# Optimization experiments

Hardware: AMD Instinct MI355X
Metric: run time of the kernel (lower is better)

Reference implementation:

```python
import jax, jax.numpy as jnp
import numpy as np

K_BITS = 128  # hash bits (k in __init__)
WORD = 32     # pack bits into uint32 words -> K_BITS // WORD = 4 words


def _pack_bits(bits_u32):
    # bits_u32: [N, K_BITS] uint32 in {0,1} -> [N, K_BITS//WORD] uint32 keys
    N = bits_u32.shape[0]
    b = bits_u32.reshape(N, K_BITS // WORD, WORD)
    shifts = jnp.arange(WORD, dtype=jnp.uint32)
    return jnp.sum(jnp.left_shift(b, shifts), axis=-1, dtype=jnp.uint32)  # [N, 4]


def setup_inputs() -> dict:
    key = jax.random.key(0)
    k1, k2 = jax.random.split(key)
    T, B, D = 128, 64, 4096
    latent_state = jax.random.normal(k1, (T, B, D), dtype=jnp.float32)
    A = jax.random.normal(k2, (K_BITS, D), dtype=jnp.float32)  # fixed random projection buffer
    return {"latent_state": latent_state, "A": A}


def reference(latent_state, A):
    # latent_state: [T, B, D]; A: [k, D]. Returns intrinsic reward [T, B].
    T, B, D = latent_state.shape
    flat = latent_state.reshape(T * B, D)                    # detach is a no-op for fwd
    proj = flat @ A.T                                        # [N, k]
    bits = (proj > 0).astype(jnp.uint32)                     # SimHash sign bits
    words = _pack_bits(bits)                                 # [N, 4] collision-free 128-bit key

    # counts dict starts empty each run: visit count of row i is the number of
    # rows j <= i with an identical key (keys processed in row order).
    N = words.shape[0]
    eq = jnp.ones((N, N), dtype=bool)
    for w in range(K_BITS // WORD):  # small fixed loop over 4 key words
        eq = eq & (words[:, None, w] == words[None, :, w])
    counts = jnp.tril(eq).sum(axis=1)                        # [N] int, >= 1
    intrinsic = 1.0 / jnp.sqrt(counts.astype(latent_state.dtype))
    return intrinsic.reshape(T, B)
```

## Files before the change

kernel.cpp:

```cpp
#include <hip/hip_runtime.h>
#include <stdint.h>

#define D_DIM 4096
#define N_ROWS 8192

typedef __attribute__((ext_vector_type(8))) short bfrag8;
typedef __attribute__((ext_vector_type(4))) float facc4;
typedef unsigned long long u64;

__device__ __forceinline__ uint32_t pack_bf16x2(float lo, float hi) {
    union { float f; uint32_t u; } a, b;
    a.f = lo; b.f = hi;
    return (b.u & 0xFFFF0000u) | (a.u >> 16);
}

__global__ void __launch_bounds__(256)
prep_A(const float* __restrict__ A, uint32_t* __restrict__ A_sw) {
    const int S = blockIdx.x * 256 + threadIdx.x;
    const int c = S >> 10;
    const int s = S & 1023;
    const int n = s >> 3;
    const int g = (s & 7) ^ (n & 7);
    const float* src = A + (size_t)n * D_DIM + c * 64 + g * 8;
    float4 f0 = *(const float4*)(src);
    float4 f1 = *(const float4*)(src + 4);
    uint4 o;
    o.x = pack_bf16x2(f0.x, f0.y);
    o.y = pack_bf16x2(f0.z, f0.w);
    o.z = pack_bf16x2(f1.x, f1.y);
    o.w = pack_bf16x2(f1.z, f1.w);
    *(uint4*)(A_sw + (size_t)S * 4) = o;
}

__global__ void __launch_bounds__(256)
gemm_split(const float* __restrict__ L, const uint32_t* __restrict__ A_sw,
           float* __restrict__ partials, int kpb) {
    __shared__ ushort Ls[32 * 72];
    __shared__ uint4 As[1024];

    const int tid  = threadIdx.x;
    const int wave = tid >> 6;
    const int lane = tid & 63;
    const int split = blockIdx.x;
    const int row0 = blockIdx.y * 32;
    const int c  = lane & 15;
    const int q  = lane >> 4;
    const int wm = wave >> 1;
    const int wn = wave & 1;

    const int lrow = tid >> 3;
    const int lf4  = tid & 7;
    const float* lsrc = L + (size_t)(row0 + lrow) * D_DIM + lf4 * 4;
    ushort* ldst = &Ls[lrow * 72 + lf4 * 4];

    facc4 acc[4];
#pragma unroll
    for (int i = 0; i < 4; i++) acc[i] = (facc4){0.f, 0.f, 0.f, 0.f};

    const int kc0 = split * kpb * 64;
    const int kc1 = kc0 + kpb * 64;
    for (int kc = kc0; kc < kc1; kc += 64) {
        const uint32_t* gA = A_sw + (size_t)(kc >> 6) * 4096;
#pragma unroll
        for (int i = 0; i < 4; i++) {
            const int slot0 = wave * 256 + i * 64;
            __builtin_amdgcn_global_load_lds(
                (const __attribute__((address_space(1))) uint32_t*)(gA + (slot0 + lane) * 4),
                (__attribute__((address_space(3))) uint32_t*)(&As[slot0]),
                16, 0, 0);
        }
        float4 f0 = *(const float4*)(lsrc + kc);
        float4 f1 = *(const float4*)(lsrc + kc + 32);
        *(uint2*)ldst        = make_uint2(pack_bf16x2(f0.x, f0.y), pack_bf16x2(f0.z, f0.w));
        *(uint2*)(ldst + 32) = make_uint2(pack_bf16x2(f1.x, f1.y), pack_bf16x2(f1.z, f1.w));
        __syncthreads();

#pragma unroll
        for (int ks = 0; ks < 2; ks++) {
            bfrag8 a = *(const bfrag8*)&Ls[(16 * wm + c) * 72 + ks * 32 + q * 8];
#pragma unroll
            for (int ct = 0; ct < 4; ct++) {
                const int n  = 64 * wn + 16 * ct + c;
                const int gl = ks * 4 + q;
                bfrag8 b = *(const bfrag8*)&As[n * 8 + (gl ^ (n & 7))];
                acc[ct] = __builtin_amdgcn_mfma_f32_16x16x32_bf16(a, b, acc[ct], 0, 0, 0);
            }
        }
        __syncthreads();
    }

    float* P = partials + ((size_t)split * N_ROWS * 128);
    const int rb = row0 + 16 * wm + 4 * q;
    const int cb = 64 * wn + c;
#pragma unroll
    for (int ct = 0; ct < 4; ct++)
#pragma unroll
        for (int r = 0; r < 4; r++)
            P[(size_t)(rb + r) * 128 + cb + 16 * ct] = acc[ct][r];
}

__global__ void __launch_bounds__(256)
reduce_pack(const float* __restrict__ partials, u64* __restrict__ folded, int S) {
    const int row  = blockIdx.x * 4 + (threadIdx.x >> 6);
    const int lane = threadIdx.x & 63;
    float s0 = 0.f, s1 = 0.f;
    for (int s = 0; s < S; s++) {
        const float* P = partials + ((size_t)s * N_ROWS * 128) + (size_t)row * 128;
        s0 += P[lane];
        s1 += P[lane + 64];
    }
    u64 b0 = __ballot(s0 > 0.0f);
    u64 b1 = __ballot(s1 > 0.0f);
    if (lane == 0) folded[row] = b0 ^ b1;
}

__global__ void __launch_bounds__(256)
gemm_pack(const float* __restrict__ L, const uint32_t* __restrict__ A_sw,
          u64* __restrict__ folded) {
    __shared__ ushort Ls[32 * 72];
    __shared__ uint4 As[1024];
    __shared__ u64 halves[2][32];

    const int tid  = threadIdx.x;
    const int wave = tid >> 6;
    const int lane = tid & 63;
    const int row0 = blockIdx.x * 32;
    const int c  = lane & 15;
    const int q  = lane >> 4;
    const int wm = wave >> 1;
    const int wn = wave & 1;

    const int lrow = tid >> 3;
    const int lf4  = tid & 7;
    const float* lsrc = L + (size_t)(row0 + lrow) * D_DIM + lf4 * 4;
    ushort* ldst = &Ls[lrow * 72 + lf4 * 4];

    facc4 acc[4];
#pragma unroll
    for (int i = 0; i < 4; i++) acc[i] = (facc4){0.f, 0.f, 0.f, 0.f};

    for (int kc = 0; kc < D_DIM; kc += 64) {
        const uint32_t* gA = A_sw + (size_t)(kc >> 6) * 4096;
#pragma unroll
        for (int i = 0; i < 4; i++) {
            const int slot0 = wave * 256 + i * 64;
            __builtin_amdgcn_global_load_lds(
                (const __attribute__((address_space(1))) uint32_t*)(gA + (slot0 + lane) * 4),
                (__attribute__((address_space(3))) uint32_t*)(&As[slot0]),
                16, 0, 0);
        }
        float4 f0 = *(const float4*)(lsrc + kc);
        float4 f1 = *(const float4*)(lsrc + kc + 32);
        *(uint2*)ldst        = make_uint2(pack_bf16x2(f0.x, f0.y), pack_bf16x2(f0.z, f0.w));
        *(uint2*)(ldst + 32) = make_uint2(pack_bf16x2(f1.x, f1.y), pack_bf16x2(f1.z, f1.w));
        __syncthreads();

#pragma unroll
        for (int ks = 0; ks < 2; ks++) {
            bfrag8 a = *(const bfrag8*)&Ls[(16 * wm + c) * 72 + ks * 32 + q * 8];
#pragma unroll
            for (int ct = 0; ct < 4; ct++) {
                const int n  = 64 * wn + 16 * ct + c;
                const int gl = ks * 4 + q;
                bfrag8 b = *(const bfrag8*)&As[n * 8 + (gl ^ (n & 7))];
                acc[ct] = __builtin_amdgcn_mfma_f32_16x16x32_bf16(a, b, acc[ct], 0, 0, 0);
            }
        }
        __syncthreads();
    }

    u64 masks[4][4];
#pragma unroll
    for (int ct = 0; ct < 4; ct++)
#pragma unroll
        for (int r = 0; r < 4; r++)
            masks[ct][r] = __ballot(acc[ct][r] > 0.0f);

    if (lane < 16) {
        const int qq = lane >> 2, r = lane & 3;
        u64 half = 0;
#pragma unroll
        for (int ct = 0; ct < 4; ct++) {
            u64 bits = (masks[ct][r] >> (16 * qq)) & 0xFFFFull;
            half |= bits << (16 * ct);
        }
        halves[wn][16 * wm + lane] = half;
    }
    __syncthreads();
    if (tid < 32)
        folded[row0 + tid] = halves[0][tid] ^ halves[1][tid];
}

__global__ void __launch_bounds__(512)
count_rows(const u64* __restrict__ folded, float* __restrict__ out) {
    __shared__ u64 K[N_ROWS];
    const int tid = threadIdx.x;
    for (int i = tid; i < N_ROWS; i += 512) K[i] = folded[i];
    __syncthreads();

    const int g    = blockIdx.x * 8 + (tid >> 6);
    const int lane = tid & 63;
    int rows[4];
    u64 my[4];
    int cnt[4] = {0, 0, 0, 0};
#pragma unroll
    for (int r = 0; r < 4; r++) {
        rows[r] = g + 2048 * r;
        my[r] = K[rows[r]];
    }
    const int maxrow = rows[3];
    for (int j = lane; j <= maxrow; j += 64) {
        u64 k = K[j];
#pragma unroll
        for (int r = 0; r < 4; r++)
            cnt[r] += (int)((j <= rows[r]) & (k == my[r]));
    }
#pragma unroll
    for (int r = 0; r < 4; r++) {
        int v = cnt[r];
#pragma unroll
        for (int o = 32; o; o >>= 1) v += __shfl_xor(v, o, 64);
        if (lane == 0) out[rows[r]] = rsqrtf((float)v);
    }
}

extern "C" void kernel_launch(void* const* d_in, const int* in_sizes, int n_in,
                              void* d_out, int out_size, void* d_ws, size_t ws_size,
                              hipStream_t stream) {
    const float* latent = (const float*)d_in[0];
    const float* A      = (const float*)d_in[1];
    float* out          = (float*)d_out;

    uint32_t* A_sw = (uint32_t*)d_ws;
    u64* folded = (u64*)((char*)d_ws + (1 << 20));
    float* partials = (float*)((char*)d_ws + (1 << 20) + (1 << 16));

    const size_t base = (1 << 20) + (1 << 16);
    const size_t per_split = (size_t)N_ROWS * 128 * sizeof(float);
    int S = 0;
    if (ws_size >= base + 8 * per_split)      S = 8;
    else if (ws_size >= base + 4 * per_split) S = 4;
    else if (ws_size >= base + 2 * per_split) S = 2;

    prep_A<<<256, 256, 0, stream>>>(A, A_sw);
    if (S > 0) {
        gemm_split<<<dim3(S, 256), 256, 0, stream>>>(latent, A_sw, partials, 64 / S);
        reduce_pack<<<2048, 256, 0, stream>>>(partials, folded, S);
    } else {
        gemm_pack<<<256, 256, 0, stream>>>(latent, A_sw, folded);
    }
    count_rows<<<256, 512, 0, stream>>>(folded, out);
}
```

Measured before the change: 225.8 us.

## Fuse split-K GEMM and reduction into one 1024-thread block with LDS reduce

Replaces the split-K GEMM, which wrote fp32 partials to global memory and needed a separate reduce_pack kernel, with one kernel per 32-row tile. Inside it, four 256-thread groups each handle a quarter of K and combine their accumulators through shared memory before packing the sign bits. This removes the partials round-trip through global memory and one kernel launch. The price is a 1024-thread block with four copies of the LDS buffers, which may limit occupancy, and only 256 blocks in the grid.

```diff
diff --git a/kernel.cpp b/kernel.cpp
--- a/kernel.cpp
+++ b/kernel.cpp
@@ -32,41 +32,41 @@
     *(uint4*)(A_sw + (size_t)S * 4) = o;
 }
 
-__global__ void __launch_bounds__(256)
-gemm_split(const float* __restrict__ L, const uint32_t* __restrict__ A_sw,
-           float* __restrict__ partials, int kpb) {
-    __shared__ ushort Ls[32 * 72];
-    __shared__ uint4 As[1024];
+__global__ void __launch_bounds__(1024, 4)
+gemm_pack_fused(const float* __restrict__ L, const uint32_t* __restrict__ A_sw,
+                u64* __restrict__ folded) {
+    __shared__ ushort Ls[4][32 * 72];
+    __shared__ uint4  As[4][1024];
+    __shared__ u64 halves[2][32];
 
     const int tid  = threadIdx.x;
-    const int wave = tid >> 6;
+    const int g    = tid >> 8;
+    const int t    = tid & 255;
+    const int wg   = t >> 6;
     const int lane = tid & 63;
-    const int split = blockIdx.x;
-    const int row0 = blockIdx.y * 32;
+    const int row0 = blockIdx.x * 32;
     const int c  = lane & 15;
     const int q  = lane >> 4;
-    const int wm = wave >> 1;
-    const int wn = wave & 1;
+    const int wm = wg >> 1;
+    const int wn = wg & 1;
 
-    const int lrow = tid >> 3;
-    const int lf4  = tid & 7;
-    const float* lsrc = L + (size_t)(row0 + lrow) * D_DIM + lf4 * 4;
-    ushort* ldst = &Ls[lrow * 72 + lf4 * 4];
+    const int lrow = t >> 3;
+    const int lf4  = t & 7;
+    const float* lsrc = L + (size_t)(row0 + lrow) * D_DIM + g * 1024 + lf4 * 4;
+    ushort* ldst = &Ls[g][lrow * 72 + lf4 * 4];
 
     facc4 acc[4];
 #pragma unroll
     for (int i = 0; i < 4; i++) acc[i] = (facc4){0.f, 0.f, 0.f, 0.f};
 
-    const int kc0 = split * kpb * 64;
-    const int kc1 = kc0 + kpb * 64;
-    for (int kc = kc0; kc < kc1; kc += 64) {
-        const uint32_t* gA = A_sw + (size_t)(kc >> 6) * 4096;
+    for (int kc = 0; kc < 1024; kc += 64) {
+        const uint32_t* gA = A_sw + (size_t)((g * 1024 + kc) >> 6) * 4096;
 #pragma unroll
         for (int i = 0; i < 4; i++) {
-            const int slot0 = wave * 256 + i * 64;
+            const int slot0 = wg * 256 + i * 64;
             __builtin_amdgcn_global_load_lds(
                 (const __attribute__((address_space(1))) uint32_t*)(gA + (slot0 + lane) * 4),
-                (__attribute__((address_space(3))) uint32_t*)(&As[slot0]),
+                (__attribute__((address_space(3))) uint32_t*)(&As[g][slot0]),
                 16, 0, 0);
         }
         float4 f0 = *(const float4*)(lsrc + kc);
@@ -77,114 +77,52 @@
 
 #pragma unroll
         for (int ks = 0; ks < 2; ks++) {
-            bfrag8 a = *(const bfrag8*)&Ls[(16 * wm + c) * 72 + ks * 32 + q * 8];
+            bfrag8 a = *(const bfrag8*)&Ls[g][(16 * wm + c) * 72 + ks * 32 + q * 8];
 #pragma unroll
             for (int ct = 0; ct < 4; ct++) {
                 const int n  = 64 * wn + 16 * ct + c;
                 const int gl = ks * 4 + q;
-                bfrag8 b = *(const bfrag8*)&As[n * 8 + (gl ^ (n & 7))];
+                bfrag8 b = *(const bfrag8*)&As[g][n * 8 + (gl ^ (n & 7))];
                 acc[ct] = __builtin_amdgcn_mfma_f32_16x16x32_bf16(a, b, acc[ct], 0, 0, 0);
             }
         }
         __syncthreads();
     }
 
-    float* P = partials + ((size_t)split * N_ROWS * 128);
-    const int rb = row0 + 16 * wm + 4 * q;
-    const int cb = 64 * wn + c;
+    facc4* red = (facc4*)&As[0][0];
+    const int sw = (t >> 1) & 7;
+    if (g > 0) {
+        facc4* dst = red + (g - 1) * 1024;
 #pragma unroll
-    for (int ct = 0; ct < 4; ct++)
+        for (int ct = 0; ct < 4; ct++)
+            dst[(t * 4 + ct) ^ sw] = acc[ct];
+    }
+    __syncthreads();
+    if (g == 0) {
 #pragma unroll
-        for (int r = 0; r < 4; r++)
-            P[(size_t)(rb + r) * 128 + cb + 16 * ct] = acc[ct][r];
-}
+        for (int s = 0; s < 3; s++) {
+            const facc4* src = red + s * 1024;
+#pragma unroll
+            for (int ct = 0; ct < 4; ct++)
+                acc[ct] += src[(t * 4 + ct) ^ sw];
+        }
+        u64 masks[4][4];
+#pragma unroll
+        for (int ct = 0; ct < 4; ct++)
+#pragma unroll
+            for (int r = 0; r < 4; r++)
+                masks[ct][r] = __ballot(acc[ct][r] > 0.0f);
 
-__global__ void __launch_bounds__(256)
-reduce_pack(const float* __restrict__ partials, u64* __restrict__ folded, int S) {
-    const int row  = blockIdx.x * 4 + (threadIdx.x >> 6);
-    const int lane = threadIdx.x & 63;
-    float s0 = 0.f, s1 = 0.f;
-    for (int s = 0; s < S; s++) {
-        const float* P = partials + ((size_t)s * N_ROWS * 128) + (size_t)row * 128;
-        s0 += P[lane];
-        s1 += P[lane + 64];
-    }
-    u64 b0 = __ballot(s0 > 0.0f);
-    u64 b1 = __ballot(s1 > 0.0f);
-    if (lane == 0) folded[row] = b0 ^ b1;
-}
-
-__global__ void __launch_bounds__(256)
-gemm_pack(const float* __restrict__ L, const uint32_t* __restrict__ A_sw,
-          u64* __restrict__ folded) {
-    __shared__ ushort Ls[32 * 72];
-    __shared__ uint4 As[1024];
-    __shared__ u64 halves[2][32];
-
-    const int tid  = threadIdx.x;
-    const int wave = tid >> 6;
-    const int lane = tid & 63;
-    const int row0 = blockIdx.x * 32;
-    const int c  = lane & 15;
-    const int q  = lane >> 4;
-    const int wm = wave >> 1;
-    const int wn = wave & 1;
-
-    const int lrow = tid >> 3;
-    const int lf4  = tid & 7;
-    const float* lsrc = L + (size_t)(row0 + lrow) * D_DIM + lf4 * 4;
-    ushort* ldst = &Ls[lrow * 72 + lf4 * 4];
-
-    facc4 acc[4];
-#pragma unroll
-    for (int i = 0; i < 4; i++) acc[i] = (facc4){0.f, 0.f, 0.f, 0.f};
-
-    for (int kc = 0; kc < D_DIM; kc += 64) {
-        const uint32_t* gA = A_sw + (size_t)(kc >> 6) * 4096;
-#pragma unroll
-        for (int i = 0; i < 4; i++) {
-            const int slot0 = wave * 256 + i * 64;
-            __builtin_amdgcn_global_load_lds(
-                (const __attribute__((address_space(1))) uint32_t*)(gA + (slot0 + lane) * 4),
-                (__attribute__((address_space(3))) uint32_t*)(&As[slot0]),
-                16, 0, 0);
-        }
-        float4 f0 = *(const float4*)(lsrc + kc);
-        float4 f1 = *(const float4*)(lsrc + kc + 32);
-        *(uint2*)ldst        = make_uint2(pack_bf16x2(f0.x, f0.y), pack_bf16x2(f0.z, f0.w));
-        *(uint2*)(ldst + 32) = make_uint2(pack_bf16x2(f1.x, f1.y), pack_bf16x2(f1.z, f1.w));
-        __syncthreads();
-
-#pragma unroll
-        for (int ks = 0; ks < 2; ks++) {
-            bfrag8 a = *(const bfrag8*)&Ls[(16 * wm + c) * 72 + ks * 32 + q * 8];
+        if (lane < 16) {
+            const int qq = lane >> 2, r = lane & 3;
+            u64 half = 0;
 #pragma unroll
             for (int ct = 0; ct < 4; ct++) {
-                const int n  = 64 * wn + 16 * ct + c;
-                const int gl = ks * 4 + q;
-                bfrag8 b = *(const bfrag8*)&As[n * 8 + (gl ^ (n & 7))];
-                acc[ct] = __builtin_amdgcn_mfma_f32_16x16x32_bf16(a, b, acc[ct], 0, 0, 0);
+                u64 bits = (masks[ct][r] >> (16 * qq)) & 0xFFFFull;
+                half |= bits << (16 * ct);
             }
+            halves[wn][16 * wm + lane] = half;
         }
-        __syncthreads();
-    }
-
-    u64 masks[4][4];
-#pragma unroll
-    for (int ct = 0; ct < 4; ct++)
-#pragma unroll
-        for (int r = 0; r < 4; r++)
-            masks[ct][r] = __ballot(acc[ct][r] > 0.0f);
-
-    if (lane < 16) {
-        const int qq = lane >> 2, r = lane & 3;
-        u64 half = 0;
-#pragma unroll
-        for (int ct = 0; ct < 4; ct++) {
-            u64 bits = (masks[ct][r] >> (16 * qq)) & 0xFFFFull;
-            half |= bits << (16 * ct);
-        }
-        halves[wn][16 * wm + lane] = half;
     }
     __syncthreads();
     if (tid < 32)
@@ -233,21 +171,8 @@
 
     uint32_t* A_sw = (uint32_t*)d_ws;
     u64* folded = (u64*)((char*)d_ws + (1 << 20));
-    float* partials = (float*)((char*)d_ws + (1 << 20) + (1 << 16));
-
-    const size_t base = (1 << 20) + (1 << 16);
-    const size_t per_split = (size_t)N_ROWS * 128 * sizeof(float);
-    int S = 0;
-    if (ws_size >= base + 8 * per_split)      S = 8;
-    else if (ws_size >= base + 4 * per_split) S = 4;
-    else if (ws_size >= base + 2 * per_split) S = 2;
 
     prep_A<<<256, 256, 0, stream>>>(A, A_sw);
-    if (S > 0) {
-        gemm_split<<<dim3(S, 256), 256, 0, stream>>>(latent, A_sw, partials, 64 / S);
-        reduce_pack<<<2048, 256, 0, stream>>>(partials, folded, S);
-    } else {
-        gemm_pack<<<256, 256, 0, stream>>>(latent, A_sw, folded);
-    }
+    gemm_pack_fused<<<256, 1024, 0, stream>>>(latent, A_sw, folded);
     count_rows<<<256, 512, 0, stream>>>(folded, out);
 }
```

Measured after the change: 228.7 us. No clear change (+1.3%).

## Enlarge split-K GEMM row tile to 128 rows to reuse A tile across rows

Applied to the files above, without the earlier changes.

The split-K projection GEMM now processes 128 latent rows per block instead of 32. Each wave computes a 4x4 grid of MFMA tiles, so every A fragment loaded from LDS is reused across four row tiles. This cuts how often the 128xK A chunk is reloaded per row, at the cost of more accumulator registers and a 4x smaller grid (S x 64 blocks), which may lower occupancy or parallelism. The fused non-split fallback is removed and S defaults to 1, so the split path always runs.

```diff
diff --git a/kernel.cpp b/kernel.cpp
--- a/kernel.cpp
+++ b/kernel.cpp
@@ -32,17 +32,17 @@
     *(uint4*)(A_sw + (size_t)S * 4) = o;
 }
 
-__global__ void __launch_bounds__(256)
-gemm_split(const float* __restrict__ L, const uint32_t* __restrict__ A_sw,
-           float* __restrict__ partials, int kpb) {
-    __shared__ ushort Ls[32 * 72];
-    __shared__ uint4 As[1024];
+__global__ void __launch_bounds__(256, 2)
+gemm_split128(const float* __restrict__ L, const uint32_t* __restrict__ A_sw,
+              float* __restrict__ partials, int kpb) {
+    __shared__ ushort Ls[128 * 72];
+    __shared__ uint4  As[1024];
 
     const int tid  = threadIdx.x;
     const int wave = tid >> 6;
     const int lane = tid & 63;
     const int split = blockIdx.x;
-    const int row0 = blockIdx.y * 32;
+    const int row0 = blockIdx.y * 128;
     const int c  = lane & 15;
     const int q  = lane >> 4;
     const int wm = wave >> 1;
@@ -53,9 +53,11 @@
     const float* lsrc = L + (size_t)(row0 + lrow) * D_DIM + lf4 * 4;
     ushort* ldst = &Ls[lrow * 72 + lf4 * 4];
 
-    facc4 acc[4];
+    facc4 acc[4][4];
 #pragma unroll
-    for (int i = 0; i < 4; i++) acc[i] = (facc4){0.f, 0.f, 0.f, 0.f};
+    for (int m = 0; m < 4; m++)
+#pragma unroll
+        for (int ct = 0; ct < 4; ct++) acc[m][ct] = (facc4){0.f, 0.f, 0.f, 0.f};
 
     const int kc0 = split * kpb * 64;
     const int kc1 = kc0 + kpb * 64;
@@ -69,34 +71,48 @@
                 (__attribute__((address_space(3))) uint32_t*)(&As[slot0]),
                 16, 0, 0);
         }
-        float4 f0 = *(const float4*)(lsrc + kc);
-        float4 f1 = *(const float4*)(lsrc + kc + 32);
-        *(uint2*)ldst        = make_uint2(pack_bf16x2(f0.x, f0.y), pack_bf16x2(f0.z, f0.w));
-        *(uint2*)(ldst + 32) = make_uint2(pack_bf16x2(f1.x, f1.y), pack_bf16x2(f1.z, f1.w));
+#pragma unroll
+        for (int i = 0; i < 4; i++) {
+            const float* p = lsrc + (size_t)i * 32 * D_DIM + kc;
+            float4 f0 = *(const float4*)(p);
+            float4 f1 = *(const float4*)(p + 32);
+            *(uint2*)(ldst + i * 32 * 72) =
+                make_uint2(pack_bf16x2(f0.x, f0.y), pack_bf16x2(f0.z, f0.w));
+            *(uint2*)(ldst + i * 32 * 72 + 32) =
+                make_uint2(pack_bf16x2(f1.x, f1.y), pack_bf16x2(f1.z, f1.w));
+        }
         __syncthreads();
 
 #pragma unroll
         for (int ks = 0; ks < 2; ks++) {
-            bfrag8 a = *(const bfrag8*)&Ls[(16 * wm + c) * 72 + ks * 32 + q * 8];
+            bfrag8 a[4];
+#pragma unroll
+            for (int m = 0; m < 4; m++)
+                a[m] = *(const bfrag8*)&Ls[(64 * wm + 16 * m + c) * 72 + ks * 32 + q * 8];
 #pragma unroll
             for (int ct = 0; ct < 4; ct++) {
                 const int n  = 64 * wn + 16 * ct + c;
                 const int gl = ks * 4 + q;
                 bfrag8 b = *(const bfrag8*)&As[n * 8 + (gl ^ (n & 7))];
-                acc[ct] = __builtin_amdgcn_mfma_f32_16x16x32_bf16(a, b, acc[ct], 0, 0, 0);
+#pragma unroll
+                for (int m = 0; m < 4; m++)
+                    acc[m][ct] = __builtin_amdgcn_mfma_f32_16x16x32_bf16(a[m], b, acc[m][ct], 0, 0, 0);
             }
         }
         __syncthreads();
     }
 
     float* P = partials + ((size_t)split * N_ROWS * 128);
-    const int rb = row0 + 16 * wm + 4 * q;
     const int cb = 64 * wn + c;
 #pragma unroll
-    for (int ct = 0; ct < 4; ct++)
+    for (int m = 0; m < 4; m++) {
+        const int rb = row0 + 64 * wm + 16 * m + 4 * q;
 #pragma unroll
-        for (int r = 0; r < 4; r++)
-            P[(size_t)(rb + r) * 128 + cb + 16 * ct] = acc[ct][r];
+        for (int ct = 0; ct < 4; ct++)
+#pragma unroll
+            for (int r = 0; r < 4; r++)
+                P[(size_t)(rb + r) * 128 + cb + 16 * ct] = acc[m][ct][r];
+    }
 }
 
 __global__ void __launch_bounds__(256)
@@ -112,83 +128,6 @@
     u64 b0 = __ballot(s0 > 0.0f);
     u64 b1 = __ballot(s1 > 0.0f);
     if (lane == 0) folded[row] = b0 ^ b1;
-}
-
-__global__ void __launch_bounds__(256)
-gemm_pack(const float* __restrict__ L, const uint32_t* __restrict__ A_sw,
-          u64* __restrict__ folded) {
-    __shared__ ushort Ls[32 * 72];
-    __shared__ uint4 As[1024];
-    __shared__ u64 halves[2][32];
-
-    const int tid  = threadIdx.x;
-    const int wave = tid >> 6;
-    const int lane = tid & 63;
-    const int row0 = blockIdx.x * 32;
-    const int c  = lane & 15;
-    const int q  = lane >> 4;
-    const int wm = wave >> 1;
-    const int wn = wave & 1;
-
-    const int lrow = tid >> 3;
-    const int lf4  = tid & 7;
-    const float* lsrc = L + (size_t)(row0 + lrow) * D_DIM + lf4 * 4;
-    ushort* ldst = &Ls[lrow * 72 + lf4 * 4];
-
-    facc4 acc[4];
-#pragma unroll
-    for (int i = 0; i < 4; i++) acc[i] = (facc4){0.f, 0.f, 0.f, 0.f};
-
-    for (int kc = 0; kc < D_DIM; kc += 64) {
-        const uint32_t* gA = A_sw + (size_t)(kc >> 6) * 4096;
-#pragma unroll
-        for (int i = 0; i < 4; i++) {
-            const int slot0 = wave * 256 + i * 64;
-            __builtin_amdgcn_global_load_lds(
-                (const __attribute__((address_space(1))) uint32_t*)(gA + (slot0 + lane) * 4),
-                (__attribute__((address_space(3))) uint32_t*)(&As[slot0]),
-                16, 0, 0);
-        }
-        float4 f0 = *(const float4*)(lsrc + kc);
-        float4 f1 = *(const float4*)(lsrc + kc + 32);
-        *(uint2*)ldst        = make_uint2(pack_bf16x2(f0.x, f0.y), pack_bf16x2(f0.z, f0.w));
-        *(uint2*)(ldst + 32) = make_uint2(pack_bf16x2(f1.x, f1.y), pack_bf16x2(f1.z, f1.w));
-        __syncthreads();
-
-#pragma unroll
-        for (int ks = 0; ks < 2; ks++) {
-            bfrag8 a = *(const bfrag8*)&Ls[(16 * wm + c) * 72 + ks * 32 + q * 8];
-#pragma unroll
-            for (int ct = 0; ct < 4; ct++) {
-                const int n  = 64 * wn + 16 * ct + c;
-                const int gl = ks * 4 + q;
-                bfrag8 b = *(const bfrag8*)&As[n * 8 + (gl ^ (n & 7))];
-                acc[ct] = __builtin_amdgcn_mfma_f32_16x16x32_bf16(a, b, acc[ct], 0, 0, 0);
-            }
-        }
-        __syncthreads();
-    }
-
-    u64 masks[4][4];
-#pragma unroll
-    for (int ct = 0; ct < 4; ct++)
-#pragma unroll
-        for (int r = 0; r < 4; r++)
-            masks[ct][r] = __ballot(acc[ct][r] > 0.0f);
-
-    if (lane < 16) {
-        const int qq = lane >> 2, r = lane & 3;
-        u64 half = 0;
-#pragma unroll
-        for (int ct = 0; ct < 4; ct++) {
-            u64 bits = (masks[ct][r] >> (16 * qq)) & 0xFFFFull;
-            half |= bits << (16 * ct);
-        }
-        halves[wn][16 * wm + lane] = half;
-    }
-    __syncthreads();
-    if (tid < 32)
-        folded[row0 + tid] = halves[0][tid] ^ halves[1][tid];
 }
 
 __global__ void __launch_bounds__(512)
@@ -237,17 +176,13 @@
 
     const size_t base = (1 << 20) + (1 << 16);
     const size_t per_split = (size_t)N_ROWS * 128 * sizeof(float);
-    int S = 0;
+    int S = 1;
     if (ws_size >= base + 8 * per_split)      S = 8;
     else if (ws_size >= base + 4 * per_split) S = 4;
     else if (ws_size >= base + 2 * per_split) S = 2;
 
     prep_A<<<256, 256, 0, stream>>>(A, A_sw);
-    if (S > 0) {
-        gemm_split<<<dim3(S, 256), 256, 0, stream>>>(latent, A_sw, partials, 64 / S);
-        reduce_pack<<<2048, 256, 0, stream>>>(partials, folded, S);
-    } else {
-        gemm_pack<<<256, 256, 0, stream>>>(latent, A_sw, folded);
-    }
+    gemm_split128<<<dim3(S, 64), 256, 0, stream>>>(latent, A_sw, partials, 64 / S);
+    reduce_pack<<<2048, 256, 0, stream>>>(partials, folded, S);
     count_rows<<<256, 512, 0, stream>>>(folded, out);
 }
```

Result: slower. 234.3 us (+3.7%).
